# Optimization experiments

Measured on AMD Instinct MI355X. Metric: run time of the kernel, lower is better.

The kernel has to match this reference:

```python
import jax, jax.numpy as jnp
import numpy as np
from jax.scipy.special import logsumexp

TAG_NAMES = ['<pad>', 'O', 'B-PER', 'I-PER', 'B-LOC', 'I-LOC', 'B-ORG', 'I-ORG', 'B-MISC', 'I-MISC']
K = len(TAG_NAMES)
T, B, D = 512, 64, 1024
PAD = 0
IMP = -100.0
VOCAB = 30000


def _crf_params(rng):
    # torchcrf reset_parameters: uniform(-0.1, 0.1), then init_crf_transitions overrides
    start = rng.uniform(-0.1, 0.1, K).astype(np.float32)
    end = rng.uniform(-0.1, 0.1, K).astype(np.float32)
    trans = rng.uniform(-0.1, 0.1, (K, K)).astype(np.float32)
    for i, name in enumerate(TAG_NAMES):
        if name[0] in ('I', 'L') or name == '<pad>':
            start[i] = IMP
        if name[0] in ('B', 'I'):
            end[i] = IMP
    tag_is = {p: [i for i, t in enumerate(TAG_NAMES) if t[0] == p] for p in 'BIOUL'}
    tag_is['P'] = [i for i, t in enumerate(TAG_NAMES) if t == 'tag']
    for ft, tos in {'B': 'BOUP', 'I': 'BOUP', 'O': 'IL', 'U': 'IL'}.items():
        for fi in tag_is[ft]:
            for tt in tos:
                for ti in tag_is[tt]:
                    trans[fi, ti] = IMP
    for ft, tos in {'B': 'IL', 'I': 'IL'}.items():
        for fi in tag_is[ft]:
            for tt in tos:
                for ti in tag_is[tt]:
                    if TAG_NAMES[fi].split('-')[1] != TAG_NAMES[ti].split('-')[1]:
                        trans[fi, ti] = IMP
    return jnp.asarray(start), jnp.asarray(end), jnp.asarray(trans)


def setup_inputs() -> dict:
    rng = np.random.default_rng(0)
    # torchcrf requires mask[0] == 1 everywhere and contiguous masks -> build from lengths
    lengths = rng.integers(T // 2, T + 1, size=B)
    valid = np.arange(T)[:, None] < lengths[None, :]  # (T, B)
    words = np.where(valid, rng.integers(1, VOCAB, size=(T, B)), PAD).astype(np.int64)
    tags = rng.integers(0, K, size=(T, B)).astype(np.int64)
    word_features = rng.standard_normal((T, B, D)).astype(np.float32)
    W = (rng.standard_normal((D, K)) / np.sqrt(D)).astype(np.float32)
    b = np.zeros(K, np.float32)
    start, end, trans = _crf_params(rng)
    return dict(words=jnp.asarray(words), tags=jnp.asarray(tags),
                word_features=jnp.asarray(word_features), W=jnp.asarray(W), b=jnp.asarray(b),
                start_trans=start, end_trans=end, transitions=trans)


def _crf_loss(emissions, tags, maskf, start, end, trans):
    """-log p(tags | emissions), summed over batch (torchcrf reduction='sum')."""
    bidx = jnp.arange(emissions.shape[1])
    # gold-path score (numerator)
    score0 = start[tags[0]] + emissions[0, bidx, tags[0]]
    em_tag = jnp.take_along_axis(emissions[1:], tags[1:, :, None], axis=-1)[..., 0]  # (T-1,B)
    step = trans[tags[:-1], tags[1:]] + em_tag
    numer = score0 + jnp.sum(step * maskf[1:], axis=0)
    seq_ends = maskf.sum(0).astype(jnp.int32) - 1
    numer = numer + end[tags[seq_ends, bidx]]
    # partition function (forward algorithm, stable log-sum-exp scan)
    def fwd_step(score, xs):
        em_t, m_t = xs
        nxt = logsumexp(score[:, :, None] + trans[None] + em_t[:, None, :], axis=1)  # (B,K)
        return jnp.where(m_t[:, None] > 0, nxt, score), None
    score, _ = jax.lax.scan(fwd_step, start[None] + emissions[0], (emissions[1:], maskf[1:]))
    denom = logsumexp(score + end[None], axis=1)
    return -(numer - denom).sum()


def _crf_decode(emissions, maskf, start, end, trans):
    """Viterbi decode; returns (T,B) int32 paths, 0-padded past sequence ends."""
    bidx = jnp.arange(emissions.shape[1])
    def vit_step(score, xs):
        em_t, m_t = xs
        bcast = score[:, :, None] + trans[None] + em_t[:, None, :]  # (B, K_prev, K_cur)
        best = bcast.max(axis=1)
        idx = bcast.argmax(axis=1).astype(jnp.int32)
        return jnp.where(m_t[:, None] > 0, best, score), idx
    score, history = jax.lax.scan(vit_step, start[None] + emissions[0], (emissions[1:], maskf[1:]))
    last_tag = jnp.argmax(score + end[None], axis=1).astype(jnp.int32)  # tag at seq_end per batch
    def back_step(tag, xs):
        hist_t, m_t = xs
        prev = jnp.where(m_t > 0, hist_t[bidx, tag], tag)
        return prev, prev
    _, path_head = jax.lax.scan(back_step, last_tag, (history, maskf[1:]), reverse=True)
    paths = jnp.concatenate([path_head, last_tag[None]], axis=0)  # (T, B)
    return jnp.where(maskf > 0, paths, 0)


def reference(words, tags, word_features, W, b, start_trans, end_trans, transitions):
    # eval-mode dropout is identity; fc projects features to tag emissions
    emissions = word_features @ W + b  # (T, B, K)
    maskf = (words != PAD).astype(emissions.dtype)  # (T, B)
    paths = _crf_decode(emissions, maskf, start_trans, end_trans, transitions)
    loss = _crf_loss(emissions, tags, maskf, start_trans, end_trans, transitions)
    return paths, loss
```

## Files before the change

kernel.cpp:

```cpp
#include <hip/hip_runtime.h>
#include <hip/hip_bf16.h>

#define TT 512
#define BB 64
#define KK 10
#define DD 1024
#define CL 32
#define NC 16

typedef unsigned char uchar;
typedef short bf16x8 __attribute__((ext_vector_type(8)));
typedef float f32x4 __attribute__((ext_vector_type(4)));

__device__ __forceinline__ unsigned f2bf(float f) {
    unsigned u = __float_as_uint(f);
    return (u + 0x7FFFu + ((u >> 16) & 1u)) >> 16;
}

__device__ __forceinline__ float max10(const float* r) {
    float m0 = fmaxf(r[0], r[1]), m1 = fmaxf(r[2], r[3]);
    float m2 = fmaxf(r[4], r[5]), m3 = fmaxf(r[6], r[7]);
    float m4 = fmaxf(r[8], r[9]);
    m0 = fmaxf(m0, m1); m2 = fmaxf(m2, m3); m0 = fmaxf(m0, m2);
    return fmaxf(m0, m4);
}

__device__ __forceinline__ float lse10(const float* r) {
    const float m = max10(r);
    float s0 = __expf(r[0] - m) + __expf(r[1] - m);
    float s1 = __expf(r[2] - m) + __expf(r[3] - m);
    float s2 = __expf(r[4] - m) + __expf(r[5] - m);
    float s3 = __expf(r[6] - m) + __expf(r[7] - m);
    float s4 = __expf(r[8] - m) + __expf(r[9] - m);
    return m + __logf(((s0 + s1) + (s2 + s3)) + s4);
}

__global__ __launch_bounds__(512) void k_emissions(
    const int* __restrict__ words, const float* __restrict__ wf,
    const float* __restrict__ W, const float* __restrict__ bias,
    float* __restrict__ em, int* __restrict__ lenArr, float* loss_slot) {
    const int tid = threadIdx.x;
    if (blockIdx.x == 256) {
        __shared__ int cnt[8][64];
        const int b = tid & 63, seg = tid >> 6;
        int c = 0;
        for (int t = seg; t < TT; t += 8) c += (words[t * BB + b] != 0) ? 1 : 0;
        cnt[seg][b] = c;
        __syncthreads();
        if (tid < 64) {
            int s = 0;
            #pragma unroll
            for (int g = 0; g < 8; ++g) s += cnt[g][tid];
            lenArr[tid] = s;
        }
        if (tid == 0) *loss_slot = 0.f;
        return;
    }

    __shared__ uint4 Bfrag[32][64];
    for (int idx = tid; idx < 32 * 64; idx += 512) {
        const int ks = idx >> 6, l = idx & 63;
        const int col = l & 15, kg = l >> 4;
        unsigned u[4];
        #pragma unroll
        for (int p = 0; p < 4; ++p) {
            unsigned lo = 0, hi = 0;
            if (col < KK) {
                const int k0 = ks * 32 + kg * 8 + p * 2;
                lo = f2bf(W[(size_t)k0 * KK + col]);
                hi = f2bf(W[(size_t)(k0 + 1) * KK + col]);
            }
            u[p] = lo | (hi << 16);
        }
        Bfrag[ks][l] = make_uint4(u[0], u[1], u[2], u[3]);
    }
    __syncthreads();

    const int wave = tid >> 6, lane = tid & 63;
    const int arow = lane & 15;
    const int kg   = lane >> 4;
    const int row0 = blockIdx.x * 128 + wave * 16;
    const float* ap = wf + (size_t)(row0 + arow) * DD + kg * 8;

    const float bk = bias[arow < KK ? arow : 0];

    f32x4 acc = {0.f, 0.f, 0.f, 0.f};
    float4 fa[4], fb[4];
    #pragma unroll
    for (int p = 0; p < 4; ++p) {
        fa[p] = *reinterpret_cast<const float4*>(ap + p * 32);
        fb[p] = *reinterpret_cast<const float4*>(ap + p * 32 + 4);
    }
    #pragma unroll
    for (int ks = 0; ks < 32; ++ks) {
        const int s = ks & 3;
        bf16x8 afr;
        afr[0] = (short)f2bf(fa[s].x); afr[1] = (short)f2bf(fa[s].y);
        afr[2] = (short)f2bf(fa[s].z); afr[3] = (short)f2bf(fa[s].w);
        afr[4] = (short)f2bf(fb[s].x); afr[5] = (short)f2bf(fb[s].y);
        afr[6] = (short)f2bf(fb[s].z); afr[7] = (short)f2bf(fb[s].w);
        union { uint4 u; bf16x8 v; } bu;
        bu.u = Bfrag[ks][lane];
        if (ks < 28) {
            fa[s] = *reinterpret_cast<const float4*>(ap + (ks + 4) * 32);
            fb[s] = *reinterpret_cast<const float4*>(ap + (ks + 4) * 32 + 4);
        }
        acc = __builtin_amdgcn_mfma_f32_16x16x32_bf16(afr, bu.v, acc, 0, 0, 0);
    }
    if (arow < KK) {
        #pragma unroll
        for (int r = 0; r < 4; ++r)
            em[(size_t)(row0 + kg * 4 + r) * KK + arow] = acc[r] + bk;
    }
}

__global__ __launch_bounds__(128) void k_chunk(
    const float* __restrict__ em, const float* __restrict__ trans,
    const int* __restrict__ lenArr, float* __restrict__ Mlse, float* __restrict__ Mmax) {
    int id = blockIdx.x;
    const bool mx = id >= 1024; id &= 1023;
    const int b = id >> 4, c = id & 15;
    const int len = lenArr[b];
    const int s_lo = c * CL + 1;
    const int s_hi = min(c * CL + CL, len - 1);
    const int ns = s_hi - s_lo + 1;
    if (ns <= 0) return;

    __shared__ float Ms[KK][12];
    __shared__ float eml[CL][KK];
    const int tid = threadIdx.x;
    for (int idx = tid; idx < CL * KK; idx += 128) {
        const int sl = idx / KK, j = idx % KK;
        const int s = s_lo + sl;
        eml[sl][j] = (s <= TT - 1) ? em[((size_t)s * BB + b) * KK + j] : 0.f;
    }
    const int i = tid / KK, j = tid % KK;
    const bool act = tid < KK * KK;
    float trc[KK];
    if (act) {
        #pragma unroll
        for (int k = 0; k < KK; ++k) trc[k] = trans[k * KK + j];
    }
    __syncthreads();
    float cur = 0.f;
    if (act) { cur = trans[i * KK + j] + eml[0][j]; Ms[i][j] = cur; }
    __syncthreads();
    for (int sl = 1; sl < ns; ++sl) {
        float row[KK];
        if (act) {
            #pragma unroll
            for (int k = 0; k < KK; ++k) row[k] = Ms[i][k] + trc[k];
        }
        __syncthreads();
        if (act) {
            cur = (mx ? max10(row) : lse10(row)) + eml[sl][j];
            Ms[i][j] = cur;
        }
        __syncthreads();
    }
    if (act) {
        float* out = mx ? Mmax : Mlse;
        out[((size_t)b * NC + c) * 100 + i * KK + j] = cur;
    }
}

__global__ __launch_bounds__(64) void k_fold(
    const int* __restrict__ tags, const float* __restrict__ em,
    const float* __restrict__ startv, const float* __restrict__ endv,
    const float* __restrict__ trans, const int* __restrict__ lenArr,
    const float* __restrict__ Mlse, const float* __restrict__ Mmax,
    float* __restrict__ ubnd, int* __restrict__ ltag, float* loss_slot) {
    const int b = blockIdx.x & 63;
    const bool mx = blockIdx.x >= 64;
    const int lane = threadIdx.x;
    const int len = lenArr[b];

    float v[KK];
    #pragma unroll
    for (int i = 0; i < KK; ++i) v[i] = startv[i] + em[(size_t)b * KK + i];

    const float* M = mx ? Mmax : Mlse;
    for (int c = 0; c < NC; ++c) {
        if (mx && lane < KK) ubnd[((size_t)b * NC + c) * KK + lane] = v[lane];
        const int s_lo = c * CL + 1;
        const int s_hi = min(c * CL + CL, len - 1);
        if (s_hi >= s_lo) {
            float nv = 0.f;
            if (lane < KK) {
                float r[KK];
                #pragma unroll
                for (int k = 0; k < KK; ++k)
                    r[k] = v[k] + M[((size_t)b * NC + c) * 100 + k * KK + lane];
                nv = mx ? max10(r) : lse10(r);
            }
            #pragma unroll
            for (int i = 0; i < KK; ++i) v[i] = __shfl(nv, i);
        }
    }

    if (mx) {
        float best = v[0] + endv[0];
        int bi = 0;
        #pragma unroll
        for (int i = 1; i < KK; ++i) {
            const float x = v[i] + endv[i];
            if (x > best) { best = x; bi = i; }
        }
        if (lane == 0) ltag[b] = bi;
    } else {
        float r[KK];
        #pragma unroll
        for (int i = 0; i < KK; ++i) r[i] = v[i] + endv[i];
        const float denom = lse10(r);
        float part = 0.f;
        for (int t = 1 + lane; t < len; t += 64) {
            const int tp = tags[(t - 1) * BB + b];
            const int tc = tags[t * BB + b];
            part += trans[tp * KK + tc] + em[((size_t)t * BB + b) * KK + tc];
        }
        #pragma unroll
        for (int off = 32; off >= 1; off >>= 1) part += __shfl_xor(part, off);
        const int t0 = tags[b];
        const int te = tags[(len - 1) * BB + b];
        const float numer = part + startv[t0] + em[(size_t)b * KK + t0] + endv[te];
        if (lane == 0) atomicAdd(loss_slot, denom - numer);
    }
}

__global__ __launch_bounds__(64) void k_hist(
    const float* __restrict__ em, const float* __restrict__ trans,
    const int* __restrict__ lenArr, const float* __restrict__ ubnd,
    int* __restrict__ Fmap, uchar* __restrict__ hist) {
    const int b = blockIdx.x >> 4, c = blockIdx.x & 15;
    const int len = lenArr[b];
    const int s_lo = c * CL + 1;
    const int s_hi = min(c * CL + CL, len - 1);
    const int ns = s_hi - s_lo + 1;
    if (ns <= 0) return;

    __shared__ float eml[CL][KK];
    __shared__ uchar hl[CL * KK];
    const int lane = threadIdx.x, j = lane;
    for (int idx = lane; idx < CL * KK; idx += 64) {
        const int sl = idx / KK, jj = idx % KK;
        const int s = s_lo + sl;
        eml[sl][jj] = (s <= TT - 1) ? em[((size_t)s * BB + b) * KK + jj] : 0.f;
    }
    float trc[KK];
    if (j < KK) {
        #pragma unroll
        for (int i = 0; i < KK; ++i) trc[i] = trans[i * KK + j];
    }
    float s[KK];
    #pragma unroll
    for (int i = 0; i < KK; ++i) s[i] = ubnd[((size_t)b * NC + c) * KK + i];
    __syncthreads();

    for (int sl = 0; sl < ns; ++sl) {
        float best = s[0] + trc[0];
        int bi = 0;
        #pragma unroll
        for (int i = 1; i < KK; ++i) {
            const float x = s[i] + trc[i];
            if (x > best) { best = x; bi = i; }
        }
        const float snew = best + eml[sl][j];
        if (j < KK) hl[sl * KK + j] = (uchar)bi;
        #pragma unroll
        for (int i = 0; i < KK; ++i) s[i] = __shfl(snew, i);
    }
    __syncthreads();
    if (j < KK) {
        int cur = j;
        for (int sl = ns - 1; sl >= 0; --sl) cur = hl[sl * KK + cur];
        Fmap[((size_t)b * NC + c) * KK + j] = cur;
    }
    __syncthreads();
    const int* hli = (const int*)&hl[0];
    int* hg = (int*)(hist + ((size_t)b * NC + c) * (CL * KK));
    for (int idx = lane; idx < CL * KK / 4; idx += 64) hg[idx] = hli[idx];
}

__global__ __launch_bounds__(1024) void k_paths(
    const int* __restrict__ lenArr, const int* __restrict__ ltag,
    const int* __restrict__ Fmap, const uchar* __restrict__ hist,
    int* __restrict__ paths) {
    const int b = blockIdx.x;
    const int len = lenArr[b];
    const int tid = threadIdx.x;
    __shared__ int Fl[NC][KK];
    __shared__ uchar hl[NC][CL * KK];
    __shared__ int vt[NC + 1];

    for (int idx = tid; idx < NC * KK; idx += 1024)
        Fl[idx / KK][idx % KK] = Fmap[(size_t)b * NC * KK + idx];
    const int* hg = (const int*)(hist + (size_t)b * NC * CL * KK);
    int* hls = (int*)&hl[0][0];
    for (int idx = tid; idx < NC * CL * KK / 4; idx += 1024) hls[idx] = hg[idx];
    __syncthreads();

    if (tid == 0) {
        int cur = ltag[b];
        vt[NC] = cur;
        for (int c = NC - 1; c >= 0; --c) {
            const int s_lo = c * CL + 1;
            const int s_hi = min(c * CL + CL, len - 1);
            if (s_hi >= s_lo) cur = Fl[c][cur];
            vt[c] = cur;
        }
    }
    __syncthreads();

    const int w = tid >> 6, lane = tid & 63;
    const int t0 = w * CL;
    if (lane < CL) {
        const int t = t0 + lane;
        if (t >= len) paths[t * BB + b] = 0;
    }
    if (lane == 0) {
        const int a = min(t0 + CL, len - 1);
        if (a >= t0) {
            int cur = vt[w + 1];
            for (int t = a; t >= t0; --t) {
                if (t <= t0 + CL - 1) paths[t * BB + b] = cur;
                if (t > t0) cur = (int)hl[w][(t - t0 - 1) * KK + cur];
            }
        }
    }
}

extern "C" void kernel_launch(void* const* d_in, const int* in_sizes, int n_in,
                              void* d_out, int out_size, void* d_ws, size_t ws_size,
                              hipStream_t stream) {
    const int*   words  = (const int*)d_in[0];
    const int*   tags   = (const int*)d_in[1];
    const float* wf     = (const float*)d_in[2];
    const float* W      = (const float*)d_in[3];
    const float* bias   = (const float*)d_in[4];
    const float* startv = (const float*)d_in[5];
    const float* endv   = (const float*)d_in[6];
    const float* trans  = (const float*)d_in[7];

    float* em   = (float*)d_ws;
    float* Mlse = em + 327680;
    float* Mmax = Mlse + 102400;
    float* ubnd = Mmax + 102400;
    int*   lenA = (int*)(ubnd + 10240);
    int*   ltag = lenA + 64;
    int*   Fmap = ltag + 64;
    uchar* hist = (uchar*)(Fmap + 10240);

    int*   paths     = (int*)d_out;
    float* loss_slot = ((float*)d_out) + TT * BB;

    k_emissions<<<257, 512, 0, stream>>>(words, wf, W, bias, em, lenA, loss_slot);
    k_chunk<<<2048, 128, 0, stream>>>(em, trans, lenA, Mlse, Mmax);
    k_fold<<<128, 64, 0, stream>>>(tags, em, startv, endv, trans, lenA, Mlse, Mmax,
                                   ubnd, ltag, loss_slot);
    k_hist<<<1024, 64, 0, stream>>>(em, trans, lenA, ubnd, Fmap, hist);
    k_paths<<<64, 1024, 0, stream>>>(lenA, ltag, Fmap, hist, paths);
}
```

Before: 81.55 us.

## Fuse fold, history and path kernels into one per-batch CRF kernel

Merges the three tail kernels (chunk-boundary fold, per-chunk Viterbi history, backtrace) into a single 1024-thread block per sequence. Intermediates (boundary scores, chunk maps, history bytes, emissions) stay in LDS instead of going through global memory, and two kernel launches are removed. The emission GEMM also double-buffers the LDS B-fragment reads in groups of eight. The cost is a serial dependency inside one block, where the max fold must finish before the 16 chunk waves can start their history pass.

```diff
diff --git a/kernel.cpp b/kernel.cpp
--- a/kernel.cpp
+++ b/kernel.cpp
@@ -81,7 +81,6 @@
     const int kg   = lane >> 4;
     const int row0 = blockIdx.x * 128 + wave * 16;
     const float* ap = wf + (size_t)(row0 + arow) * DD + kg * 8;
-
     const float bk = bias[arow < KK ? arow : 0];
 
     f32x4 acc = {0.f, 0.f, 0.f, 0.f};
@@ -91,21 +90,35 @@
         fa[p] = *reinterpret_cast<const float4*>(ap + p * 32);
         fb[p] = *reinterpret_cast<const float4*>(ap + p * 32 + 4);
     }
+    uint4 bcur[8], bnxt[8];
     #pragma unroll
-    for (int ks = 0; ks < 32; ++ks) {
-        const int s = ks & 3;
-        bf16x8 afr;
-        afr[0] = (short)f2bf(fa[s].x); afr[1] = (short)f2bf(fa[s].y);
-        afr[2] = (short)f2bf(fa[s].z); afr[3] = (short)f2bf(fa[s].w);
-        afr[4] = (short)f2bf(fb[s].x); afr[5] = (short)f2bf(fb[s].y);
-        afr[6] = (short)f2bf(fb[s].z); afr[7] = (short)f2bf(fb[s].w);
-        union { uint4 u; bf16x8 v; } bu;
-        bu.u = Bfrag[ks][lane];
-        if (ks < 28) {
-            fa[s] = *reinterpret_cast<const float4*>(ap + (ks + 4) * 32);
-            fb[s] = *reinterpret_cast<const float4*>(ap + (ks + 4) * 32 + 4);
-        }
-        acc = __builtin_amdgcn_mfma_f32_16x16x32_bf16(afr, bu.v, acc, 0, 0, 0);
+    for (int q = 0; q < 8; ++q) bcur[q] = Bfrag[q][lane];
+
+    #pragma unroll
+    for (int ph = 0; ph < 4; ++ph) {
+        if (ph < 3) {
+            #pragma unroll
+            for (int q = 0; q < 8; ++q) bnxt[q] = Bfrag[(ph + 1) * 8 + q][lane];
+        }
+        #pragma unroll
+        for (int q = 0; q < 8; ++q) {
+            const int ks = ph * 8 + q;
+            const int s = ks & 3;
+            bf16x8 afr;
+            afr[0] = (short)f2bf(fa[s].x); afr[1] = (short)f2bf(fa[s].y);
+            afr[2] = (short)f2bf(fa[s].z); afr[3] = (short)f2bf(fa[s].w);
+            afr[4] = (short)f2bf(fb[s].x); afr[5] = (short)f2bf(fb[s].y);
+            afr[6] = (short)f2bf(fb[s].z); afr[7] = (short)f2bf(fb[s].w);
+            if (ks < 28) {
+                fa[s] = *reinterpret_cast<const float4*>(ap + (ks + 4) * 32);
+                fb[s] = *reinterpret_cast<const float4*>(ap + (ks + 4) * 32 + 4);
+            }
+            union { uint4 u; bf16x8 v; } bu;
+            bu.u = bcur[q];
+            acc = __builtin_amdgcn_mfma_f32_16x16x32_bf16(afr, bu.v, acc, 0, 0, 0);
+        }
+        #pragma unroll
+        for (int q = 0; q < 8; ++q) bcur[q] = bnxt[q];
     }
     if (arow < KK) {
         #pragma unroll
@@ -164,41 +177,59 @@
     }
 }
 
-__global__ __launch_bounds__(64) void k_fold(
+__global__ __launch_bounds__(1024) void k_crf(
     const int* __restrict__ tags, const float* __restrict__ em,
     const float* __restrict__ startv, const float* __restrict__ endv,
     const float* __restrict__ trans, const int* __restrict__ lenArr,
     const float* __restrict__ Mlse, const float* __restrict__ Mmax,
-    float* __restrict__ ubnd, int* __restrict__ ltag, float* loss_slot) {
-    const int b = blockIdx.x & 63;
-    const bool mx = blockIdx.x >= 64;
-    const int lane = threadIdx.x;
+    int* __restrict__ paths, float* __restrict__ loss_slot) {
+    const int b = blockIdx.x;
+    const int tid = threadIdx.x;
+    const int wv = tid >> 6, lane = tid & 63;
     const int len = lenArr[b];
 
-    float v[KK];
-    #pragma unroll
-    for (int i = 0; i < KK; ++i) v[i] = startv[i] + em[(size_t)b * KK + i];
-
-    const float* M = mx ? Mmax : Mlse;
-    for (int c = 0; c < NC; ++c) {
-        if (mx && lane < KK) ubnd[((size_t)b * NC + c) * KK + lane] = v[lane];
-        const int s_lo = c * CL + 1;
-        const int s_hi = min(c * CL + CL, len - 1);
-        if (s_hi >= s_lo) {
-            float nv = 0.f;
-            if (lane < KK) {
-                float r[KK];
-                #pragma unroll
-                for (int k = 0; k < KK; ++k)
-                    r[k] = v[k] + M[((size_t)b * NC + c) * 100 + k * KK + lane];
-                nv = mx ? max10(r) : lse10(r);
-            }
-            #pragma unroll
-            for (int i = 0; i < KK; ++i) v[i] = __shfl(nv, i);
-        }
-    }
-
-    if (mx) {
+    __shared__ float Ml[NC][100];
+    __shared__ float Mm[NC][100];
+    __shared__ float eml[NC][CL][KK];
+    __shared__ float ub[NC][KK];
+    __shared__ uchar hl[NC][CL * KK];
+    __shared__ int   Fl[NC][KK];
+    __shared__ int   vt[NC + 1];
+    __shared__ float em0[KK];
+    __shared__ float red[2];
+
+    for (int idx = tid; idx < NC * 100; idx += 1024) {
+        Ml[idx / 100][idx % 100] = Mlse[(size_t)b * NC * 100 + idx];
+        Mm[idx / 100][idx % 100] = Mmax[(size_t)b * NC * 100 + idx];
+    }
+    for (int idx = tid; idx < NC * CL * KK; idx += 1024) {
+        const int c = idx / (CL * KK), r = idx % (CL * KK);
+        const int sl = r / KK, j = r % KK;
+        const int s = c * CL + 1 + sl;
+        eml[c][sl][j] = (s <= TT - 1) ? em[((size_t)s * BB + b) * KK + j] : 0.f;
+    }
+    if (tid < KK) em0[tid] = em[(size_t)b * KK + tid];
+    __syncthreads();
+
+    if (wv == 0) {
+        float v[KK];
+        #pragma unroll
+        for (int i = 0; i < KK; ++i) v[i] = startv[i] + em0[i];
+        for (int c = 0; c < NC; ++c) {
+            if (lane < KK) ub[c][lane] = v[lane];
+            const int s_hi = min(c * CL + CL, len - 1);
+            if (s_hi >= c * CL + 1) {
+                float nv = 0.f;
+                if (lane < KK) {
+                    float r[KK];
+                    #pragma unroll
+                    for (int k = 0; k < KK; ++k) r[k] = v[k] + Mm[c][k * KK + lane];
+                    nv = max10(r);
+                }
+                #pragma unroll
+                for (int i = 0; i < KK; ++i) v[i] = __shfl(nv, i);
+            }
+        }
         float best = v[0] + endv[0];
         int bi = 0;
         #pragma unroll
@@ -206,113 +237,96 @@
             const float x = v[i] + endv[i];
             if (x > best) { best = x; bi = i; }
         }
-        if (lane == 0) ltag[b] = bi;
-    } else {
+        if (lane == 0) vt[NC] = bi;
+    } else if (wv == 1) {
+        float v[KK];
+        #pragma unroll
+        for (int i = 0; i < KK; ++i) v[i] = startv[i] + em0[i];
+        for (int c = 0; c < NC; ++c) {
+            const int s_hi = min(c * CL + CL, len - 1);
+            if (s_hi >= c * CL + 1) {
+                float nv = 0.f;
+                if (lane < KK) {
+                    float r[KK];
+                    #pragma unroll
+                    for (int k = 0; k < KK; ++k) r[k] = v[k] + Ml[c][k * KK + lane];
+                    nv = lse10(r);
+                }
+                #pragma unroll
+                for (int i = 0; i < KK; ++i) v[i] = __shfl(nv, i);
+            }
+        }
         float r[KK];
         #pragma unroll
         for (int i = 0; i < KK; ++i) r[i] = v[i] + endv[i];
-        const float denom = lse10(r);
+        if (lane == 0) red[0] = lse10(r);
+    } else if (wv == 2) {
         float part = 0.f;
         for (int t = 1 + lane; t < len; t += 64) {
             const int tp = tags[(t - 1) * BB + b];
             const int tc = tags[t * BB + b];
-            part += trans[tp * KK + tc] + em[((size_t)t * BB + b) * KK + tc];
+            part += trans[tp * KK + tc] + eml[(t - 1) >> 5][(t - 1) & 31][tc];
         }
         #pragma unroll
         for (int off = 32; off >= 1; off >>= 1) part += __shfl_xor(part, off);
-        const int t0 = tags[b];
-        const int te = tags[(len - 1) * BB + b];
-        const float numer = part + startv[t0] + em[(size_t)b * KK + t0] + endv[te];
-        if (lane == 0) atomicAdd(loss_slot, denom - numer);
-    }
-}
-
-__global__ __launch_bounds__(64) void k_hist(
-    const float* __restrict__ em, const float* __restrict__ trans,
-    const int* __restrict__ lenArr, const float* __restrict__ ubnd,
-    int* __restrict__ Fmap, uchar* __restrict__ hist) {
-    const int b = blockIdx.x >> 4, c = blockIdx.x & 15;
-    const int len = lenArr[b];
-    const int s_lo = c * CL + 1;
-    const int s_hi = min(c * CL + CL, len - 1);
-    const int ns = s_hi - s_lo + 1;
-    if (ns <= 0) return;
-
-    __shared__ float eml[CL][KK];
-    __shared__ uchar hl[CL * KK];
-    const int lane = threadIdx.x, j = lane;
-    for (int idx = lane; idx < CL * KK; idx += 64) {
-        const int sl = idx / KK, jj = idx % KK;
-        const int s = s_lo + sl;
-        eml[sl][jj] = (s <= TT - 1) ? em[((size_t)s * BB + b) * KK + jj] : 0.f;
-    }
-    float trc[KK];
-    if (j < KK) {
-        #pragma unroll
-        for (int i = 0; i < KK; ++i) trc[i] = trans[i * KK + j];
-    }
-    float s[KK];
-    #pragma unroll
-    for (int i = 0; i < KK; ++i) s[i] = ubnd[((size_t)b * NC + c) * KK + i];
-    __syncthreads();
-
-    for (int sl = 0; sl < ns; ++sl) {
-        float best = s[0] + trc[0];
-        int bi = 0;
-        #pragma unroll
-        for (int i = 1; i < KK; ++i) {
-            const float x = s[i] + trc[i];
-            if (x > best) { best = x; bi = i; }
-        }
-        const float snew = best + eml[sl][j];
-        if (j < KK) hl[sl * KK + j] = (uchar)bi;
-        #pragma unroll
-        for (int i = 0; i < KK; ++i) s[i] = __shfl(snew, i);
-    }
-    __syncthreads();
-    if (j < KK) {
-        int cur = j;
-        for (int sl = ns - 1; sl >= 0; --sl) cur = hl[sl * KK + cur];
-        Fmap[((size_t)b * NC + c) * KK + j] = cur;
-    }
-    __syncthreads();
-    const int* hli = (const int*)&hl[0];
-    int* hg = (int*)(hist + ((size_t)b * NC + c) * (CL * KK));
-    for (int idx = lane; idx < CL * KK / 4; idx += 64) hg[idx] = hli[idx];
-}
-
-__global__ __launch_bounds__(1024) void k_paths(
-    const int* __restrict__ lenArr, const int* __restrict__ ltag,
-    const int* __restrict__ Fmap, const uchar* __restrict__ hist,
-    int* __restrict__ paths) {
-    const int b = blockIdx.x;
-    const int len = lenArr[b];
-    const int tid = threadIdx.x;
-    __shared__ int Fl[NC][KK];
-    __shared__ uchar hl[NC][CL * KK];
-    __shared__ int vt[NC + 1];
-
-    for (int idx = tid; idx < NC * KK; idx += 1024)
-        Fl[idx / KK][idx % KK] = Fmap[(size_t)b * NC * KK + idx];
-    const int* hg = (const int*)(hist + (size_t)b * NC * CL * KK);
-    int* hls = (int*)&hl[0][0];
-    for (int idx = tid; idx < NC * CL * KK / 4; idx += 1024) hls[idx] = hg[idx];
+        if (lane == 0) {
+            const int t0 = tags[b];
+            const int te = tags[(len - 1) * BB + b];
+            red[1] = part + startv[t0] + em0[t0] + endv[te];
+        }
+    }
+    __syncthreads();
+
+    {
+        const int c = wv;
+        const int s_hi = min(c * CL + CL, len - 1);
+        const int ns = s_hi - (c * CL + 1) + 1;
+        if (ns > 0) {
+            float trc[KK];
+            if (lane < KK) {
+                #pragma unroll
+                for (int i = 0; i < KK; ++i) trc[i] = trans[i * KK + lane];
+            }
+            float s[KK];
+            #pragma unroll
+            for (int i = 0; i < KK; ++i) s[i] = ub[c][i];
+            for (int sl = 0; sl < ns; ++sl) {
+                float best = s[0] + trc[0];
+                int bi = 0;
+                #pragma unroll
+                for (int i = 1; i < KK; ++i) {
+                    const float x = s[i] + trc[i];
+                    if (x > best) { best = x; bi = i; }
+                }
+                float snew = 0.f;
+                if (lane < KK) {
+                    snew = best + eml[c][sl][lane];
+                    hl[c][sl * KK + lane] = (uchar)bi;
+                }
+                #pragma unroll
+                for (int i = 0; i < KK; ++i) s[i] = __shfl(snew, i);
+            }
+            if (lane < KK) {
+                int cur = lane;
+                for (int sl = ns - 1; sl >= 0; --sl) cur = hl[c][sl * KK + cur];
+                Fl[c][lane] = cur;
+            }
+        }
+    }
     __syncthreads();
 
     if (tid == 0) {
-        int cur = ltag[b];
-        vt[NC] = cur;
+        int cur = vt[NC];
         for (int c = NC - 1; c >= 0; --c) {
-            const int s_lo = c * CL + 1;
             const int s_hi = min(c * CL + CL, len - 1);
-            if (s_hi >= s_lo) cur = Fl[c][cur];
+            if (s_hi >= c * CL + 1) cur = Fl[c][cur];
             vt[c] = cur;
         }
-    }
-    __syncthreads();
-
-    const int w = tid >> 6, lane = tid & 63;
-    const int t0 = w * CL;
+        atomicAdd(loss_slot, red[0] - red[1]);
+    }
+    __syncthreads();
+
+    const int t0 = wv * CL;
     if (lane < CL) {
         const int t = t0 + lane;
         if (t >= len) paths[t * BB + b] = 0;
@@ -320,10 +334,10 @@
     if (lane == 0) {
         const int a = min(t0 + CL, len - 1);
         if (a >= t0) {
-            int cur = vt[w + 1];
+            int cur = vt[wv + 1];
             for (int t = a; t >= t0; --t) {
                 if (t <= t0 + CL - 1) paths[t * BB + b] = cur;
-                if (t > t0) cur = (int)hl[w][(t - t0 - 1) * KK + cur];
+                if (t > t0) cur = (int)hl[wv][(t - t0 - 1) * KK + cur];
             }
         }
     }
@@ -344,19 +358,13 @@
     float* em   = (float*)d_ws;
     float* Mlse = em + 327680;
     float* Mmax = Mlse + 102400;
-    float* ubnd = Mmax + 102400;
-    int*   lenA = (int*)(ubnd + 10240);
-    int*   ltag = lenA + 64;
-    int*   Fmap = ltag + 64;
-    uchar* hist = (uchar*)(Fmap + 10240);
+    int*   lenA = (int*)(Mmax + 102400);
 
     int*   paths     = (int*)d_out;
     float* loss_slot = ((float*)d_out) + TT * BB;
 
     k_emissions<<<257, 512, 0, stream>>>(words, wf, W, bias, em, lenA, loss_slot);
     k_chunk<<<2048, 128, 0, stream>>>(em, trans, lenA, Mlse, Mmax);
-    k_fold<<<128, 64, 0, stream>>>(tags, em, startv, endv, trans, lenA, Mlse, Mmax,
-                                   ubnd, ltag, loss_slot);
-    k_hist<<<1024, 64, 0, stream>>>(em, trans, lenA, ubnd, Fmap, hist);
-    k_paths<<<64, 1024, 0, stream>>>(lenA, ltag, Fmap, hist, paths);
-}
+    k_crf<<<64, 1024, 0, stream>>>(tags, em, startv, endv, trans, lenA,
+                                   Mlse, Mmax, paths, loss_slot);
+}
```

Result: faster. 78.58 us (-3.6%).
